# Kernel tuning notes

Hardware: AMD Instinct MI355X
Metric: run time of the kernel (lower is better)

The kernel has to match this reference:

```python
import jax, jax.numpy as jnp
import numpy as np

B, N, DIM, H, DH = 16, 1024, 512, 8, 64
SCALE = DH ** -0.5


def setup_inputs() -> dict:
    key = jax.random.key(0)
    ks = jax.random.split(key, 6)
    s = 0.02
    return {
        "x": jax.random.normal(ks[0], (B, N, DIM), jnp.float32),
        "pos_bias": jax.random.normal(ks[1], (H, N, N), jnp.float32),
        "Wq": jax.random.normal(ks[2], (DIM, DIM), jnp.float32) * s,
        "Wk": jax.random.normal(ks[3], (DIM, DIM), jnp.float32) * s,
        "Wv": jax.random.normal(ks[4], (DIM, DIM), jnp.float32) * s,
        "Wo": jax.random.normal(ks[5], (DIM, DIM), jnp.float32) * s,
    }


def reference(x, pos_bias, Wq, Wk, Wv, Wo):
    b, n, _ = x.shape
    # bias-free Linear: y = x @ W.T
    q = (x @ Wq.T).reshape(b, n, H, DH).transpose(0, 2, 1, 3)  # b h n d
    k = (x @ Wk.T).reshape(b, n, H, DH).transpose(0, 2, 1, 3)
    v = (x @ Wv.T).reshape(b, n, H, DH).transpose(0, 2, 1, 3)
    q = q * SCALE
    sim = jnp.einsum("bhid,bhjd->bhij", q, k) + pos_bias[None]  # b h n n
    attn = jax.nn.softmax(sim, axis=-1)
    out = jnp.einsum("bhij,bhjd->bhid", attn, v)
    out = out.transpose(0, 2, 1, 3).reshape(b, n, H * DH)
    return out @ Wo.T
```

## Files before the change

kernel.cpp:

```cpp
#include <hip/hip_runtime.h>

typedef unsigned int u32;
typedef unsigned short u16;
typedef __bf16 bf16x8 __attribute__((ext_vector_type(8)));
typedef __attribute__((ext_vector_type(4))) float f32x4;

#define MFMA16(a, b, c) __builtin_amdgcn_mfma_f32_16x16x32_bf16((a), (b), (c), 0, 0, 0)

static constexpr int SEQ = 1024, DIM = 512, NH = 8;

__device__ __forceinline__ u16 f2bf(float f) {
  u32 b = __float_as_uint(f);
  return (u16)((b + 0x7FFFu + ((b >> 16) & 1u)) >> 16);
}

__device__ __forceinline__ void g2l16(const void* g, void* l) {
  __builtin_amdgcn_global_load_lds(
      (const __attribute__((address_space(1))) u32*)g,
      (__attribute__((address_space(3))) u32*)l, 16, 0, 0);
}

__device__ __forceinline__ bf16x8 ldsr8(const u16* base, int row, int slot) {
  int phys = slot ^ (row & 7);
  return *(const bf16x8*)(base + row * 64 + phys * 8);
}

__global__ void cvt4(const float4* __restrict__ src, ushort4* __restrict__ dst, int n4) {
  int stride = gridDim.x * blockDim.x;
  for (int i = blockIdx.x * blockDim.x + threadIdx.x; i < n4; i += stride) {
    float4 v = src[i];
    ushort4 o;
    o.x = f2bf(v.x); o.y = f2bf(v.y); o.z = f2bf(v.z); o.w = f2bf(v.w);
    dst[i] = o;
  }
}

__global__ __launch_bounds__(256)
void transpose_v(const u16* __restrict__ Vw, u16* __restrict__ Vt) {
  __shared__ u16 t[64][80];
  const int ct = blockIdx.x;
  const int nt = blockIdx.y;
  const int b  = blockIdx.z;
  const int tid = threadIdx.x;

#pragma unroll
  for (int p = 0; p < 2; ++p) {
    int id = tid + p * 256;
    int row = id >> 3, ch = id & 7;
    bf16x8 v = *(const bf16x8*)(Vw + (size_t)(b * 1024 + nt * 64 + row) * 512 + ct * 64 + ch * 8);
    const u16* u = (const u16*)&v;
#pragma unroll
    for (int j = 0; j < 8; ++j) t[ch * 8 + j][row] = u[j];
  }
  __syncthreads();
#pragma unroll
  for (int p = 0; p < 2; ++p) {
    int id = tid + p * 256;
    int row = id >> 3, ch = id & 7;
    bf16x8 v = *(const bf16x8*)&t[row][ch * 8];
    *(bf16x8*)(Vt + (size_t)(b * 512 + ct * 64 + row) * 1024 + nt * 64 + ch * 8) = v;
  }
}

template <int OUT_F32>
__global__ __launch_bounds__(256)
void gemm_bt(const u16* __restrict__ A,
             const u16* __restrict__ B0, const u16* __restrict__ B1, const u16* __restrict__ B2,
             void* __restrict__ D0, void* __restrict__ D1, void* __restrict__ D2,
             float scale0) {
  __shared__ u16 As[128 * 64];
  __shared__ u16 Bs[128 * 64];

  const int tid = threadIdx.x;
  const int w = tid >> 6, l = tid & 63;
  const int sel = blockIdx.x >> 2;
  const u16* Bw = (sel == 0) ? B0 : ((sel == 1) ? B1 : B2);
  void* Dv = (sel == 0) ? D0 : ((sel == 1) ? D1 : D2);
  const float scale = (sel == 0) ? scale0 : 1.0f;
  const int n0 = (blockIdx.x & 3) * 128;
  const int m0 = blockIdx.y * 128;

  const int srow = l >> 3;
  const int sslot = (l & 7) ^ srow;
  const int wr = w >> 1, wc = w & 1;

  f32x4 acc[4][4] = {};

  for (int kk = 0; kk < 512; kk += 64) {
#pragma unroll
    for (int it = 0; it < 4; ++it) {
      int row = w * 32 + it * 8;
      g2l16(A + (size_t)(m0 + row + srow) * 512 + kk + sslot * 8, &As[row * 64]);
      g2l16(Bw + (size_t)(n0 + row + srow) * 512 + kk + sslot * 8, &Bs[row * 64]);
    }
    __syncthreads();

#pragma unroll
    for (int ks = 0; ks < 2; ++ks) {
      int slot = ks * 4 + (l >> 4);
      bf16x8 af[4], bfr[4];
#pragma unroll
      for (int m = 0; m < 4; ++m) af[m] = ldsr8(As, wr * 64 + m * 16 + (l & 15), slot);
#pragma unroll
      for (int n = 0; n < 4; ++n) bfr[n] = ldsr8(Bs, wc * 64 + n * 16 + (l & 15), slot);
#pragma unroll
      for (int m = 0; m < 4; ++m)
#pragma unroll
        for (int n = 0; n < 4; ++n)
          acc[m][n] = MFMA16(af[m], bfr[n], acc[m][n]);
    }
    __syncthreads();
  }

#pragma unroll
  for (int m = 0; m < 4; ++m) {
    int row = m0 + wr * 64 + m * 16 + ((l >> 4) << 2);
#pragma unroll
    for (int n = 0; n < 4; ++n) {
      int col = n0 + wc * 64 + n * 16 + (l & 15);
#pragma unroll
      for (int r = 0; r < 4; ++r) {
        float v = acc[m][n][r] * scale;
        if (OUT_F32)
          ((float*)Dv)[(size_t)(row + r) * 512 + col] = v;
        else
          ((u16*)Dv)[(size_t)(row + r) * 512 + col] = f2bf(v);
      }
    }
  }
}

__device__ __forceinline__ void attn_iter(
    int kt, const u16* Kc, const u16* Vc, u16* Kn, u16* Vn,
    const float (&bcur)[16], float (&bnxt)[16],
    const u16* __restrict__ K, const u16* __restrict__ Vt,
    const float* bbase, int b, int h, int w, int l, int srow, int sslot,
    const bf16x8 (&qf)[2], u16* Pw, f32x4 (&o_acc)[4], float (&ps)[4]) {
  const bool notlast = (kt < 15);

  if (notlast) {
#pragma unroll
    for (int it = 0; it < 2; ++it) {
      int row = w * 16 + it * 8;
      g2l16(K + (size_t)(b * SEQ + (kt + 1) * 64 + row + srow) * DIM + h * 64 + sslot * 8,
            &Kn[row * 64]);
      g2l16(Vt + (size_t)(b * 512 + h * 64 + row + srow) * SEQ + (kt + 1) * 64 + sslot * 8,
            &Vn[row * 64]);
    }
  }

  f32x4 sacc[4];
#pragma unroll
  for (int nf = 0; nf < 4; ++nf)
#pragma unroll
    for (int r = 0; r < 4; ++r) sacc[nf][r] = bcur[nf * 4 + r];
#pragma unroll
  for (int ks = 0; ks < 2; ++ks) {
    int slot = ks * 4 + (l >> 4);
#pragma unroll
    for (int nf = 0; nf < 4; ++nf) {
      bf16x8 kf = ldsr8(Kc, nf * 16 + (l & 15), slot);
      sacc[nf] = MFMA16(qf[ks], kf, sacc[nf]);
    }
  }

  if (notlast) {
#pragma unroll
    for (int i = 0; i < 16; ++i)
      bnxt[i] = bbase[(size_t)(i & 3) * SEQ + (kt + 1) * 64 + (i >> 2) * 16];
  }

#pragma unroll
  for (int r = 0; r < 4; ++r) {
    int prow = ((l >> 4) << 2) + r;
#pragma unroll
    for (int nf = 0; nf < 4; ++nf) {
      float p = __expf(sacc[nf][r]);
      ps[r] += p;
      int col = nf * 16 + (l & 15);
      int slot = (col >> 3) ^ (prow & 7);
      Pw[prow * 64 + slot * 8 + (col & 7)] = f2bf(p);
    }
  }

#pragma unroll
  for (int ks = 0; ks < 2; ++ks) {
    bf16x8 pf = ldsr8(Pw, l & 15, ks * 4 + (l >> 4));
    int slot = ks * 4 + (l >> 4);
#pragma unroll
    for (int nf = 0; nf < 4; ++nf) {
      bf16x8 vf = ldsr8(Vc, nf * 16 + (l & 15), slot);
      o_acc[nf] = MFMA16(pf, vf, o_acc[nf]);
    }
  }
  __syncthreads();
}

__global__ __launch_bounds__(256, 4)
void attn_kern(const u16* __restrict__ Q, const u16* __restrict__ K,
               const u16* __restrict__ Vt, const float* __restrict__ bias,
               u16* __restrict__ O) {
  __shared__ u16 QPs[64 * 64];
  __shared__ u16 K0s[64 * 64], V0s[64 * 64], K1s[64 * 64], V1s[64 * 64];

  const int tid = threadIdx.x;
  const int w = tid >> 6, l = tid & 63;
  const int b = blockIdx.x, h = blockIdx.y, qt = blockIdx.z;

  const int srow = l >> 3;
  const int sslot = (l & 7) ^ srow;

#pragma unroll
  for (int it = 0; it < 2; ++it) {
    int row = w * 16 + it * 8;
    g2l16(Q + (size_t)(b * SEQ + qt * 64 + row + srow) * DIM + h * 64 + sslot * 8,
          &QPs[row * 64]);
    g2l16(K + (size_t)(b * SEQ + row + srow) * DIM + h * 64 + sslot * 8, &K0s[row * 64]);
    g2l16(Vt + (size_t)(b * 512 + h * 64 + row + srow) * SEQ + sslot * 8, &V0s[row * 64]);
  }
  const int qrow0 = qt * 64 + w * 16 + ((l >> 4) << 2);
  const float* bbase = bias + ((size_t)h * SEQ + qrow0) * SEQ + (l & 15);
  float biasA[16], biasB[16];
#pragma unroll
  for (int i = 0; i < 16; ++i) biasA[i] = bbase[(size_t)(i & 3) * SEQ + (i >> 2) * 16];
  __syncthreads();

  bf16x8 qf[2];
#pragma unroll
  for (int ks = 0; ks < 2; ++ks)
    qf[ks] = ldsr8(QPs, w * 16 + (l & 15), ks * 4 + (l >> 4));
  u16* Pw = &QPs[w * 16 * 64];

  f32x4 o_acc[4] = {};
  float ps[4] = {};

  for (int kt = 0; kt < 16; kt += 2) {
    attn_iter(kt, K0s, V0s, K1s, V1s, biasA, biasB, K, Vt, bbase,
              b, h, w, l, srow, sslot, qf, Pw, o_acc, ps);
    attn_iter(kt + 1, K1s, V1s, K0s, V0s, biasB, biasA, K, Vt, bbase,
              b, h, w, l, srow, sslot, qf, Pw, o_acc, ps);
  }

  float rinv[4];
#pragma unroll
  for (int r = 0; r < 4; ++r) {
    float s = ps[r];
    s += __shfl_xor(s, 1); s += __shfl_xor(s, 2);
    s += __shfl_xor(s, 4); s += __shfl_xor(s, 8);
    rinv[r] = 1.0f / s;
  }
  const int orow0 = b * SEQ + qt * 64 + w * 16 + ((l >> 4) << 2);
#pragma unroll
  for (int nf = 0; nf < 4; ++nf) {
    int col = h * 64 + nf * 16 + (l & 15);
#pragma unroll
    for (int r = 0; r < 4; ++r)
      O[(size_t)(orow0 + r) * DIM + col] = f2bf(o_acc[nf][r] * rinv[r]);
  }
}

extern "C" void kernel_launch(void* const* d_in, const int* in_sizes, int n_in,
                              void* d_out, int out_size, void* d_ws, size_t ws_size,
                              hipStream_t stream) {
  const float* x  = (const float*)d_in[0];
  const float* pb = (const float*)d_in[1];
  const float* Wq = (const float*)d_in[2];
  const float* Wk = (const float*)d_in[3];
  const float* Wv = (const float*)d_in[4];
  const float* Wo = (const float*)d_in[5];

  const size_t MR = (size_t)16384 * 512;

  u16* Qw = (u16*)d_out;
  u16* Kw = Qw + MR;

  char* ws = (char*)d_ws;
  u16* slot0 = (u16*)ws; ws += MR * 2;
  u16* slot1 = (u16*)ws; ws += MR * 2;
  u16* wqb = (u16*)ws; ws += 512 * 512 * 2;
  u16* wkb = (u16*)ws; ws += 512 * 512 * 2;
  u16* wvb = (u16*)ws; ws += 512 * 512 * 2;
  u16* wob = (u16*)ws; ws += 512 * 512 * 2;

  u16* xb = slot0;
  u16* Vw = slot1;
  u16* Vt = slot0;
  u16* AO = slot1;

  cvt4<<<2048, 256, 0, stream>>>((const float4*)x, (ushort4*)xb, (int)(MR / 4));
  cvt4<<<256, 256, 0, stream>>>((const float4*)Wq, (ushort4*)wqb, 512 * 512 / 4);
  cvt4<<<256, 256, 0, stream>>>((const float4*)Wk, (ushort4*)wkb, 512 * 512 / 4);
  cvt4<<<256, 256, 0, stream>>>((const float4*)Wv, (ushort4*)wvb, 512 * 512 / 4);
  cvt4<<<256, 256, 0, stream>>>((const float4*)Wo, (ushort4*)wob, 512 * 512 / 4);

  gemm_bt<0><<<dim3(12, 128), 256, 0, stream>>>(xb, wqb, wkb, wvb, Qw, Kw, Vw, 0.125f);

  transpose_v<<<dim3(8, 16, 16), 256, 0, stream>>>(Vw, Vt);

  attn_kern<<<dim3(16, NH, 16), 256, 0, stream>>>(Qw, Kw, Vt, pb, AO);

  gemm_bt<1><<<dim3(4, 128), 256, 0, stream>>>(AO, wob, wob, wob, d_out, d_out, d_out, 1.0f);
}
```

Baseline: 263.2 us.

## Enlarge attention query tile to 128 rows with 8 waves sharing K/V tiles

The attention kernel now runs 512 threads (8 waves) per block covering 128 query rows, so each K/V tile loaded into shared memory serves twice as many queries. Each wave now stages 8 rows instead of 16. MFMA sections are wrapped in s_setprio to favour matrix issue. The four weight conversion launches are merged into one launch, cutting launch overhead. The larger block raises LDS and register pressure per block and halves the grid size, which may reduce occupancy and latency hiding.

Result: slower. 513.5 us (+95.1%).

```diff
diff --git a/kernel.cpp b/kernel.cpp
--- a/kernel.cpp
+++ b/kernel.cpp
@@ -32,6 +32,24 @@
     ushort4 o;
     o.x = f2bf(v.x); o.y = f2bf(v.y); o.z = f2bf(v.z); o.w = f2bf(v.w);
     dst[i] = o;
+  }
+}
+
+__global__ __launch_bounds__(256)
+void cvtw(const float4* __restrict__ a, const float4* __restrict__ b,
+          const float4* __restrict__ c, const float4* __restrict__ d,
+          ushort4* __restrict__ oa, ushort4* __restrict__ ob,
+          ushort4* __restrict__ oc, ushort4* __restrict__ od) {
+  const int which = blockIdx.y;
+  const float4* s = (which == 0) ? a : (which == 1) ? b : (which == 2) ? c : d;
+  ushort4* o = (which == 0) ? oa : (which == 1) ? ob : (which == 2) ? oc : od;
+  const int n4 = 512 * 512 / 4;
+  int stride = gridDim.x * blockDim.x;
+  for (int i = blockIdx.x * blockDim.x + threadIdx.x; i < n4; i += stride) {
+    float4 v = s[i];
+    ushort4 t;
+    t.x = f2bf(v.x); t.y = f2bf(v.y); t.z = f2bf(v.z); t.w = f2bf(v.w);
+    o[i] = t;
   }
 }
 
@@ -139,14 +157,11 @@
   const bool notlast = (kt < 15);
 
   if (notlast) {
-#pragma unroll
-    for (int it = 0; it < 2; ++it) {
-      int row = w * 16 + it * 8;
-      g2l16(K + (size_t)(b * SEQ + (kt + 1) * 64 + row + srow) * DIM + h * 64 + sslot * 8,
-            &Kn[row * 64]);
-      g2l16(Vt + (size_t)(b * 512 + h * 64 + row + srow) * SEQ + (kt + 1) * 64 + sslot * 8,
-            &Vn[row * 64]);
-    }
+    int row = w * 8;
+    g2l16(K + (size_t)(b * SEQ + (kt + 1) * 64 + row + srow) * DIM + h * 64 + sslot * 8,
+          &Kn[row * 64]);
+    g2l16(Vt + (size_t)(b * 512 + h * 64 + row + srow) * SEQ + (kt + 1) * 64 + sslot * 8,
+          &Vn[row * 64]);
   }
 
   f32x4 sacc[4];
@@ -154,6 +169,7 @@
   for (int nf = 0; nf < 4; ++nf)
 #pragma unroll
     for (int r = 0; r < 4; ++r) sacc[nf][r] = bcur[nf * 4 + r];
+  __builtin_amdgcn_s_setprio(1);
 #pragma unroll
   for (int ks = 0; ks < 2; ++ks) {
     int slot = ks * 4 + (l >> 4);
@@ -163,6 +179,7 @@
       sacc[nf] = MFMA16(qf[ks], kf, sacc[nf]);
     }
   }
+  __builtin_amdgcn_s_setprio(0);
 
   if (notlast) {
 #pragma unroll
@@ -183,6 +200,7 @@
     }
   }
 
+  __builtin_amdgcn_s_setprio(1);
 #pragma unroll
   for (int ks = 0; ks < 2; ++ks) {
     bf16x8 pf = ldsr8(Pw, l & 15, ks * 4 + (l >> 4));
@@ -193,14 +211,15 @@
       o_acc[nf] = MFMA16(pf, vf, o_acc[nf]);
     }
   }
+  __builtin_amdgcn_s_setprio(0);
   __syncthreads();
 }
 
-__global__ __launch_bounds__(256, 4)
+__global__ __launch_bounds__(512, 6)
 void attn_kern(const u16* __restrict__ Q, const u16* __restrict__ K,
                const u16* __restrict__ Vt, const float* __restrict__ bias,
                u16* __restrict__ O) {
-  __shared__ u16 QPs[64 * 64];
+  __shared__ u16 QPs[128 * 64];
   __shared__ u16 K0s[64 * 64], V0s[64 * 64], K1s[64 * 64], V1s[64 * 64];
 
   const int tid = threadIdx.x;
@@ -213,12 +232,15 @@
 #pragma unroll
   for (int it = 0; it < 2; ++it) {
     int row = w * 16 + it * 8;
-    g2l16(Q + (size_t)(b * SEQ + qt * 64 + row + srow) * DIM + h * 64 + sslot * 8,
+    g2l16(Q + (size_t)(b * SEQ + qt * 128 + row + srow) * DIM + h * 64 + sslot * 8,
           &QPs[row * 64]);
+  }
+  {
+    int row = w * 8;
     g2l16(K + (size_t)(b * SEQ + row + srow) * DIM + h * 64 + sslot * 8, &K0s[row * 64]);
     g2l16(Vt + (size_t)(b * 512 + h * 64 + row + srow) * SEQ + sslot * 8, &V0s[row * 64]);
   }
-  const int qrow0 = qt * 64 + w * 16 + ((l >> 4) << 2);
+  const int qrow0 = qt * 128 + w * 16 + ((l >> 4) << 2);
   const float* bbase = bias + ((size_t)h * SEQ + qrow0) * SEQ + (l & 15);
   float biasA[16], biasB[16];
 #pragma unroll
@@ -249,7 +271,7 @@
     s += __shfl_xor(s, 4); s += __shfl_xor(s, 8);
     rinv[r] = 1.0f / s;
   }
-  const int orow0 = b * SEQ + qt * 64 + w * 16 + ((l >> 4) << 2);
+  const int orow0 = b * SEQ + qt * 128 + w * 16 + ((l >> 4) << 2);
 #pragma unroll
   for (int nf = 0; nf < 4; ++nf) {
     int col = h * 64 + nf * 16 + (l & 15);
@@ -288,16 +310,16 @@
   u16* AO = slot1;
 
   cvt4<<<2048, 256, 0, stream>>>((const float4*)x, (ushort4*)xb, (int)(MR / 4));
-  cvt4<<<256, 256, 0, stream>>>((const float4*)Wq, (ushort4*)wqb, 512 * 512 / 4);
-  cvt4<<<256, 256, 0, stream>>>((const float4*)Wk, (ushort4*)wkb, 512 * 512 / 4);
-  cvt4<<<256, 256, 0, stream>>>((const float4*)Wv, (ushort4*)wvb, 512 * 512 / 4);
-  cvt4<<<256, 256, 0, stream>>>((const float4*)Wo, (ushort4*)wob, 512 * 512 / 4);
+  cvtw<<<dim3(64, 4), 256, 0, stream>>>((const float4*)Wq, (const float4*)Wk,
+                                        (const float4*)Wv, (const float4*)Wo,
+                                        (ushort4*)wqb, (ushort4*)wkb,
+                                        (ushort4*)wvb, (ushort4*)wob);
 
   gemm_bt<0><<<dim3(12, 128), 256, 0, stream>>>(xb, wqb, wkb, wvb, Qw, Kw, Vw, 0.125f);
 
   transpose_v<<<dim3(8, 16, 16), 256, 0, stream>>>(Vw, Vt);
 
-  attn_kern<<<dim3(16, NH, 16), 256, 0, stream>>>(Qw, Kw, Vt, pb, AO);
+  attn_kern<<<dim3(16, NH, 8), 512, 0, stream>>>(Qw, Kw, Vt, pb, AO);
 
   gemm_bt<1><<<dim3(4, 128), 256, 0, stream>>>(AO, wob, wob, wob, d_out, d_out, d_out, 1.0f);
 }
```
